# Performance work log

Hardware: AMD Instinct MI355X
Metric: run time of the kernel (lower is better)

The kernel has to match this reference:

```python
import jax, jax.numpy as jnp
import numpy as np

NEG_SLOPE = 0.2
EPS = 1e-16
N_NODES = 50000
N_EDGES = 800000
D_IN = 128
D_E = 64
HEADS = 4
D_OUT = 32


def setup_inputs() -> dict:
    key = jax.random.key(0)
    k1, k2, k3, k4, k5, k6 = jax.random.split(key, 6)
    H = jax.random.normal(k1, (N_NODES, D_IN), dtype=jnp.float32)
    edge_index = jax.random.randint(k2, (2, N_EDGES), 0, N_NODES, dtype=jnp.int64)
    E = jax.random.normal(k3, (N_EDGES, D_E), dtype=jnp.float32)
    # torch nn.Linear weights: [out_features, in_features]
    W = jax.random.normal(k4, (HEADS * D_OUT, D_IN), dtype=jnp.float32) * (1.0 / np.sqrt(D_IN))
    W_e = jax.random.normal(k5, (HEADS * D_OUT, D_E), dtype=jnp.float32) * (1.0 / np.sqrt(D_E))
    att = jax.random.normal(k6, (1, HEADS, D_OUT), dtype=jnp.float32) * 0.1
    return {"H": H, "edge_index": edge_index, "E": E, "W": W, "W_e": W_e, "att": att}


def reference(H, edge_index, E, W, W_e, att):
    n_nodes = H.shape[0]
    # node transform: [N, heads, d_out]
    HT = (H @ W.T).reshape(n_nodes, HEADS, D_OUT)
    src, dst = edge_index[0], edge_index[1]
    # edge transform: [E, heads, d_out]
    ET = (E @ W_e.T).reshape(-1, HEADS, D_OUT)
    alpha_in = HT[src] + HT[dst] + ET              # [E, heads, d_out]
    alpha_in = jax.nn.leaky_relu(alpha_in, NEG_SLOPE)
    alpha = jnp.sum(alpha_in * att, axis=-1)        # [E, heads]
    # segment softmax over incoming edges of each dst node
    a_max = jax.ops.segment_max(alpha, dst, num_segments=n_nodes)   # [N, heads]
    alpha = jnp.exp(alpha - a_max[dst])
    a_sum = jax.ops.segment_sum(alpha, dst, num_segments=n_nodes)   # [N, heads]
    alpha = alpha / (a_sum[dst] + EPS)
    # weighted aggregation of source features
    messages = HT[src] * alpha[:, :, None]          # [E, heads, d_out]
    H_out = jax.ops.segment_sum(messages, dst, num_segments=n_nodes)  # [N, heads, d_out]
    return H_out.reshape(n_nodes, HEADS * D_OUT)    # concat=True
```

## Files before the change

kernel.cpp:

```cpp
#include <hip/hip_runtime.h>

#define N_NODES 50000
#define N_EDGES 800000
#define D_IN    128
#define D_E     64
#define NH      4
#define F_TOT   128
#define NEG_SLOPE 0.2f

typedef __attribute__((ext_vector_type(8))) short short8;
typedef __attribute__((ext_vector_type(4))) float f32x4;

__device__ __forceinline__ short f2bf(float x) {
    unsigned u = __float_as_uint(x);
    u += 0x7FFFu + ((u >> 16) & 1u);
    return (short)(u >> 16);
}

__global__ __launch_bounds__(256) void k_node_transform(
    const float* __restrict__ H, const float* __restrict__ W,
    float* __restrict__ HT)
{
    __shared__ float wt[D_IN * F_TOT];
    const int tid = threadIdx.x;
    for (int i = tid; i < D_IN * F_TOT; i += 256) {
        const int f = i & 127, k = i >> 7;
        wt[k * F_TOT + f] = W[f * D_IN + k];
    }
    __syncthreads();

    const int l = tid & 63;
    const int w = tid >> 6;
    const int gwave  = blockIdx.x * 4 + w;
    const int nwaves = gridDim.x * 4;
    const int ngroups = N_NODES / 8;

    for (int grp = gwave; grp < ngroups; grp += nwaves) {
        const int g = grp * 8;
        float ax[8], ay[8];
#pragma unroll
        for (int j = 0; j < 8; ++j) { ax[j] = 0.f; ay[j] = 0.f; }

        for (int k4 = 0; k4 < D_IN / 4; ++k4) {
            float hv[8][4];
#pragma unroll
            for (int j = 0; j < 8; ++j)
                *(float4*)hv[j] = *(const float4*)&H[(size_t)(g + j) * D_IN + k4 * 4];
#pragma unroll
            for (int kk = 0; kk < 4; ++kk) {
                const float2 wk = *(const float2*)&wt[(k4 * 4 + kk) * F_TOT + 2 * l];
#pragma unroll
                for (int j = 0; j < 8; ++j) {
                    ax[j] = fmaf(wk.x, hv[j][kk], ax[j]);
                    ay[j] = fmaf(wk.y, hv[j][kk], ay[j]);
                }
            }
        }
#pragma unroll
        for (int j = 0; j < 8; ++j) {
            float2 r; r.x = ax[j]; r.y = ay[j];
            *(float2*)&HT[(size_t)(g + j) * F_TOT + 2 * l] = r;
        }
    }
}

__global__ __launch_bounds__(256) void k_hist(
    const int* __restrict__ EI, int* __restrict__ deg)
{
    const int e = blockIdx.x * 256 + threadIdx.x;
    if (e < N_EDGES) atomicAdd(&deg[EI[N_EDGES + e]], 1);
}

__global__ __launch_bounds__(1024) void k_scan(
    const int* __restrict__ deg, int* __restrict__ row_start,
    int* __restrict__ cursor)
{
    __shared__ int wsum[16];
    __shared__ int carry;
    const int tid = threadIdx.x;
    const int l = tid & 63;
    const int wv = tid >> 6;
    if (tid == 0) carry = 0;

    for (int base = 0; base < N_NODES; base += 1024) {
        __syncthreads();
        const int cb = carry;
        const int i = base + tid;
        const int v = (i < N_NODES) ? deg[i] : 0;
        int x = v;
#pragma unroll
        for (int off = 1; off < 64; off <<= 1) {
            int t = __shfl_up(x, off, 64);
            if (l >= off) x += t;
        }
        if (l == 63) wsum[wv] = x;
        __syncthreads();
        int wave_off = 0;
        for (int k = 0; k < wv; ++k) wave_off += wsum[k];
        int tot = 0;
#pragma unroll
        for (int k = 0; k < 16; ++k) tot += wsum[k];
        const int excl = cb + wave_off + (x - v);
        if (i < N_NODES) { row_start[i] = excl; cursor[i] = excl; }
        __syncthreads();
        if (tid == 0) carry = cb + tot;
    }
    __syncthreads();
    if (tid == 0) row_start[N_NODES] = carry;
}

__global__ __launch_bounds__(256, 3) void k_logits(
    const float* __restrict__ E, const int* __restrict__ EI,
    const float* __restrict__ We, const float* __restrict__ att,
    const float* __restrict__ HT,
    float* __restrict__ wperm, int* __restrict__ srcperm,
    int* __restrict__ cursor)
{
    const int tid = threadIdx.x;
    const int l   = tid & 63;
    const int wv  = tid >> 6;
    const int r16 = l & 15;
    const int g4  = l >> 4;

    short8 bf[8][2];
#pragma unroll
    for (int ft = 0; ft < 8; ++ft) {
#pragma unroll
        for (int kc = 0; kc < 2; ++kc) {
            const float* wp = &We[(size_t)(ft * 16 + r16) * D_E + kc * 32 + g4 * 8];
            const float4 lo = *(const float4*)wp;
            const float4 hi = *(const float4*)(wp + 4);
            short8 b;
            b[0] = f2bf(lo.x); b[1] = f2bf(lo.y); b[2] = f2bf(lo.z); b[3] = f2bf(lo.w);
            b[4] = f2bf(hi.x); b[5] = f2bf(hi.y); b[6] = f2bf(hi.z); b[7] = f2bf(hi.w);
            bf[ft][kc] = b;
        }
    }
    float attv[8];
#pragma unroll
    for (int ft = 0; ft < 8; ++ft) attv[ft] = att[ft * 16 + r16];

    const int gwave  = blockIdx.x * 4 + wv;
    const int nwaves = gridDim.x * 4;
    const int ntiles = N_EDGES / 16;

    for (int t = gwave; t < ntiles; t += nwaves) {
        const int e0 = t * 16;
        short8 af[2];
#pragma unroll
        for (int kc = 0; kc < 2; ++kc) {
            const float* ep = &E[(size_t)(e0 + r16) * D_E + kc * 32 + g4 * 8];
            const float4 lo = *(const float4*)ep;
            const float4 hi = *(const float4*)(ep + 4);
            short8 a;
            a[0] = f2bf(lo.x); a[1] = f2bf(lo.y); a[2] = f2bf(lo.z); a[3] = f2bf(lo.w);
            a[4] = f2bf(hi.x); a[5] = f2bf(hi.y); a[6] = f2bf(hi.z); a[7] = f2bf(hi.w);
            af[kc] = a;
        }
        f32x4 acc[8];
#pragma unroll
        for (int ft = 0; ft < 8; ++ft) {
            f32x4 z = {0.f, 0.f, 0.f, 0.f};
            z = __builtin_amdgcn_mfma_f32_16x16x32_bf16(af[0], bf[ft][0], z, 0, 0, 0);
            acc[ft] = __builtin_amdgcn_mfma_f32_16x16x32_bf16(af[1], bf[ft][1], z, 0, 0, 0);
        }
        int sr_[4], dr_[4];
#pragma unroll
        for (int r = 0; r < 4; ++r) {
            sr_[r] = EI[e0 + g4 * 4 + r];
            dr_[r] = EI[N_EDGES + e0 + g4 * 4 + r];
        }
#pragma unroll
        for (int r = 0; r < 4; ++r) {
            const int sr = sr_[r], dr = dr_[r];
            float ph[4] = {0.f, 0.f, 0.f, 0.f};
#pragma unroll
            for (int ft = 0; ft < 8; ++ft) {
                const float hs = HT[(size_t)sr * F_TOT + ft * 16 + r16];
                const float hd = HT[(size_t)dr * F_TOT + ft * 16 + r16];
                float v = hs + hd + acc[ft][r];
                v = v > 0.f ? v : NEG_SLOPE * v;
                ph[ft >> 1] = fmaf(v, attv[ft], ph[ft >> 1]);
            }
#pragma unroll
            for (int m = 1; m < 16; m <<= 1) {
#pragma unroll
                for (int hh = 0; hh < 4; ++hh)
                    ph[hh] += __shfl_xor(ph[hh], m, 64);
            }
            const float w0 = __expf(ph[0]), w1 = __expf(ph[1]);
            const float w2 = __expf(ph[2]), w3 = __expf(ph[3]);
            int pos = 0;
            if (r16 == 0) pos = atomicAdd(&cursor[dr], 1);
            pos = __shfl(pos, l & 48, 64);
            if (r16 < 4) {
                const float wv_ = r16 == 0 ? w0 : r16 == 1 ? w1 : r16 == 2 ? w2 : w3;
                wperm[4 * pos + r16] = wv_;
            }
            if (r16 == 4) srcperm[pos] = sr;
        }
    }
}

__global__ __launch_bounds__(256, 8) void k_aggregate(
    const float* __restrict__ HT, const float* __restrict__ wperm,
    const int* __restrict__ srcperm, const int* __restrict__ row_start,
    float* __restrict__ out)
{
    const int tid = threadIdx.x;
    const int l = tid & 63;
    const int wv = tid >> 6;
    const int n = blockIdx.x * 4 + wv;
    if (n >= N_NODES) return;
    const int h = l >> 4;
    const int beg = row_start[n];
    const int end = row_start[n + 1];

    float ax = 0.f, ay = 0.f, sw = 0.f;
    for (int base = beg; base < end; base += 16) {
        const int   svl = (l < 16 && base + l < end) ? srcperm[base + l] : 0;
        const float wvl = (4 * base + l < 4 * end) ? wperm[4 * base + l] : 0.f;
#pragma unroll
        for (int j = 0; j < 16; ++j) {
            const int   s = __shfl(svl, j, 64);
            const float w = __shfl(wvl, 4 * j + h, 64);
            const float2 hs = *(const float2*)&HT[(size_t)s * F_TOT + 2 * l];
            ax = fmaf(w, hs.x, ax);
            ay = fmaf(w, hs.y, ay);
            sw += w;
        }
    }
    const float inv = 1.f / (sw + 1e-16f);
    float2 r; r.x = ax * inv; r.y = ay * inv;
    *(float2*)&out[(size_t)n * F_TOT + 2 * l] = r;
}

extern "C" void kernel_launch(void* const* d_in, const int* in_sizes, int n_in,
                              void* d_out, int out_size, void* d_ws, size_t ws_size,
                              hipStream_t stream)
{
    const float* H   = (const float*)d_in[0];
    const int*   EI  = (const int*)d_in[1];
    const float* E   = (const float*)d_in[2];
    const float* W   = (const float*)d_in[3];
    const float* We  = (const float*)d_in[4];
    const float* att = (const float*)d_in[5];
    float* out = (float*)d_out;

    float* HT        = (float*)d_ws;
    float* wperm     = HT + (size_t)N_NODES * F_TOT;
    int*   srcperm   = (int*)(wperm + (size_t)N_EDGES * NH);
    int*   deg       = srcperm + N_EDGES;
    int*   row_start = deg + N_NODES;
    int*   cursor    = row_start + N_NODES + 1;

    hipMemsetAsync(deg, 0, N_NODES * sizeof(int), stream);

    k_hist<<<(N_EDGES + 255) / 256, 256, 0, stream>>>(EI, deg);
    k_scan<<<1, 1024, 0, stream>>>(deg, row_start, cursor);
    k_node_transform<<<512, 256, 0, stream>>>(H, W, HT);
    k_logits<<<1024, 256, 0, stream>>>(E, EI, We, att, HT,
                                       wperm, srcperm, cursor);
    k_aggregate<<<(N_NODES + 3) / 4, 256, 0, stream>>>(HT, wperm, srcperm,
                                                       row_start, out);
}
```

Measured before the change: 687.3 us.

## Fuse edge logits and aggregation into per-destination-node kernel with swizzled HT

Edges are now bucketed by destination in a separate permute kernel that stores source and edge ids. A single per-node kernel then computes the edge transform via MFMA, the logits, the exponentials and the weighted aggregation, so the wperm buffer and the second gather of HT are gone. HT columns are stored in a swizzled order so each lane loads 8 contiguous floats with vector loads, and the destination row is loaded once per node. The trade-off is that E rows are now gathered in random order, degree imbalance across waves, and MFMA tiles are partly wasted on nodes whose degree is not a multiple of 16.

```diff
diff --git a/kernel.cpp b/kernel.cpp
--- a/kernel.cpp
+++ b/kernel.cpp
@@ -19,13 +19,14 @@
 
 __global__ __launch_bounds__(256) void k_node_transform(
     const float* __restrict__ H, const float* __restrict__ W,
-    float* __restrict__ HT)
+    float* __restrict__ HTsw)
 {
     __shared__ float wt[D_IN * F_TOT];
     const int tid = threadIdx.x;
     for (int i = tid; i < D_IN * F_TOT; i += 256) {
-        const int f = i & 127, k = i >> 7;
-        wt[k * F_TOT + f] = W[f * D_IN + k];
+        const int s = i & 127, k = i >> 7;
+        const int f = (s & 7) * 16 + (s >> 3);
+        wt[k * F_TOT + s] = W[f * D_IN + k];
     }
     __syncthreads();
 
@@ -59,7 +60,7 @@
 #pragma unroll
         for (int j = 0; j < 8; ++j) {
             float2 r; r.x = ax[j]; r.y = ay[j];
-            *(float2*)&HT[(size_t)(g + j) * F_TOT + 2 * l] = r;
+            *(float2*)&HTsw[(size_t)(g + j) * F_TOT + 2 * l] = r;
         }
     }
 }
@@ -109,12 +110,25 @@
     if (tid == 0) row_start[N_NODES] = carry;
 }
 
-__global__ __launch_bounds__(256, 3) void k_logits(
-    const float* __restrict__ E, const int* __restrict__ EI,
-    const float* __restrict__ We, const float* __restrict__ att,
-    const float* __restrict__ HT,
-    float* __restrict__ wperm, int* __restrict__ srcperm,
-    int* __restrict__ cursor)
+__global__ __launch_bounds__(256) void k_permute(
+    const int* __restrict__ EI, int* __restrict__ cursor,
+    int* __restrict__ srcperm, int* __restrict__ eidperm)
+{
+    const int e = blockIdx.x * 256 + threadIdx.x;
+    if (e < N_EDGES) {
+        const int s = EI[e];
+        const int d = EI[N_EDGES + e];
+        const int pos = atomicAdd(&cursor[d], 1);
+        srcperm[pos] = s;
+        eidperm[pos] = e;
+    }
+}
+
+__global__ __launch_bounds__(256, 3) void k_gat(
+    const float* __restrict__ E, const float* __restrict__ We,
+    const float* __restrict__ att, const float* __restrict__ HTsw,
+    const int* __restrict__ srcperm, const int* __restrict__ eidperm,
+    const int* __restrict__ row_start, float* __restrict__ out)
 {
     const int tid = threadIdx.x;
     const int l   = tid & 63;
@@ -140,45 +154,74 @@
 #pragma unroll
     for (int ft = 0; ft < 8; ++ft) attv[ft] = att[ft * 16 + r16];
 
-    const int gwave  = blockIdx.x * 4 + wv;
-    const int nwaves = gridDim.x * 4;
-    const int ntiles = N_EDGES / 16;
-
-    for (int t = gwave; t < ntiles; t += nwaves) {
-        const int e0 = t * 16;
-        short8 af[2];
-#pragma unroll
-        for (int kc = 0; kc < 2; ++kc) {
-            const float* ep = &E[(size_t)(e0 + r16) * D_E + kc * 32 + g4 * 8];
-            const float4 lo = *(const float4*)ep;
-            const float4 hi = *(const float4*)(ep + 4);
-            short8 a;
-            a[0] = f2bf(lo.x); a[1] = f2bf(lo.y); a[2] = f2bf(lo.z); a[3] = f2bf(lo.w);
-            a[4] = f2bf(hi.x); a[5] = f2bf(hi.y); a[6] = f2bf(hi.z); a[7] = f2bf(hi.w);
-            af[kc] = a;
-        }
+    const int n = blockIdx.x * 4 + wv;
+    if (n >= N_NODES) return;
+    const int beg = row_start[n];
+    const int end = row_start[n + 1];
+
+    float hdv[8];
+    {
+        const float4 d0 = *(const float4*)&HTsw[(size_t)n * F_TOT + r16 * 8];
+        const float4 d1 = *(const float4*)&HTsw[(size_t)n * F_TOT + r16 * 8 + 4];
+        hdv[0] = d0.x; hdv[1] = d0.y; hdv[2] = d0.z; hdv[3] = d0.w;
+        hdv[4] = d1.x; hdv[5] = d1.y; hdv[6] = d1.z; hdv[7] = d1.w;
+    }
+
+    float macc[8];
+#pragma unroll
+    for (int ft = 0; ft < 8; ++ft) macc[ft] = 0.f;
+    float sw4[4] = {0.f, 0.f, 0.f, 0.f};
+
+    for (int base = beg; base < end; base += 16) {
+        int svl = 0, evl = 0;
+        if (l < 16) {
+            const int idx = base + l;
+            const int cidx = idx < end ? idx : beg;
+            svl = srcperm[cidx];
+            evl = eidperm[cidx];
+        }
+        const int eid = __shfl(evl, r16, 64);
+        const float* ep = &E[(size_t)eid * D_E + g4 * 8];
+        const float4 a0 = *(const float4*)ep;
+        const float4 a1 = *(const float4*)(ep + 4);
+        const float4 a2 = *(const float4*)(ep + 32);
+        const float4 a3 = *(const float4*)(ep + 36);
+
+        int sidx[4];
+#pragma unroll
+        for (int r = 0; r < 4; ++r) sidx[r] = __shfl(svl, g4 * 4 + r, 64);
+        float4 h0[4], h1[4];
+#pragma unroll
+        for (int r = 0; r < 4; ++r) {
+            const float* hp = &HTsw[(size_t)sidx[r] * F_TOT + r16 * 8];
+            h0[r] = *(const float4*)hp;
+            h1[r] = *(const float4*)(hp + 4);
+        }
+
+        short8 af0, af1;
+        af0[0] = f2bf(a0.x); af0[1] = f2bf(a0.y); af0[2] = f2bf(a0.z); af0[3] = f2bf(a0.w);
+        af0[4] = f2bf(a1.x); af0[5] = f2bf(a1.y); af0[6] = f2bf(a1.z); af0[7] = f2bf(a1.w);
+        af1[0] = f2bf(a2.x); af1[1] = f2bf(a2.y); af1[2] = f2bf(a2.z); af1[3] = f2bf(a2.w);
+        af1[4] = f2bf(a3.x); af1[5] = f2bf(a3.y); af1[6] = f2bf(a3.z); af1[7] = f2bf(a3.w);
+
         f32x4 acc[8];
 #pragma unroll
         for (int ft = 0; ft < 8; ++ft) {
             f32x4 z = {0.f, 0.f, 0.f, 0.f};
-            z = __builtin_amdgcn_mfma_f32_16x16x32_bf16(af[0], bf[ft][0], z, 0, 0, 0);
-            acc[ft] = __builtin_amdgcn_mfma_f32_16x16x32_bf16(af[1], bf[ft][1], z, 0, 0, 0);
-        }
-        int sr_[4], dr_[4];
+            z = __builtin_amdgcn_mfma_f32_16x16x32_bf16(af0, bf[ft][0], z, 0, 0, 0);
+            acc[ft] = __builtin_amdgcn_mfma_f32_16x16x32_bf16(af1, bf[ft][1], z, 0, 0, 0);
+        }
+
 #pragma unroll
         for (int r = 0; r < 4; ++r) {
-            sr_[r] = EI[e0 + g4 * 4 + r];
-            dr_[r] = EI[N_EDGES + e0 + g4 * 4 + r];
-        }
-#pragma unroll
-        for (int r = 0; r < 4; ++r) {
-            const int sr = sr_[r], dr = dr_[r];
+            const bool valid = (base + g4 * 4 + r) < end;
+            float hsv[8];
+            hsv[0] = h0[r].x; hsv[1] = h0[r].y; hsv[2] = h0[r].z; hsv[3] = h0[r].w;
+            hsv[4] = h1[r].x; hsv[5] = h1[r].y; hsv[6] = h1[r].z; hsv[7] = h1[r].w;
             float ph[4] = {0.f, 0.f, 0.f, 0.f};
 #pragma unroll
             for (int ft = 0; ft < 8; ++ft) {
-                const float hs = HT[(size_t)sr * F_TOT + ft * 16 + r16];
-                const float hd = HT[(size_t)dr * F_TOT + ft * 16 + r16];
-                float v = hs + hd + acc[ft][r];
+                float v = hsv[ft] + hdv[ft] + acc[ft][r];
                 v = v > 0.f ? v : NEG_SLOPE * v;
                 ph[ft >> 1] = fmaf(v, attv[ft], ph[ft >> 1]);
             }
@@ -188,51 +231,29 @@
                 for (int hh = 0; hh < 4; ++hh)
                     ph[hh] += __shfl_xor(ph[hh], m, 64);
             }
-            const float w0 = __expf(ph[0]), w1 = __expf(ph[1]);
-            const float w2 = __expf(ph[2]), w3 = __expf(ph[3]);
-            int pos = 0;
-            if (r16 == 0) pos = atomicAdd(&cursor[dr], 1);
-            pos = __shfl(pos, l & 48, 64);
-            if (r16 < 4) {
-                const float wv_ = r16 == 0 ? w0 : r16 == 1 ? w1 : r16 == 2 ? w2 : w3;
-                wperm[4 * pos + r16] = wv_;
-            }
-            if (r16 == 4) srcperm[pos] = sr;
-        }
-    }
-}
-
-__global__ __launch_bounds__(256, 8) void k_aggregate(
-    const float* __restrict__ HT, const float* __restrict__ wperm,
-    const int* __restrict__ srcperm, const int* __restrict__ row_start,
-    float* __restrict__ out)
-{
-    const int tid = threadIdx.x;
-    const int l = tid & 63;
-    const int wv = tid >> 6;
-    const int n = blockIdx.x * 4 + wv;
-    if (n >= N_NODES) return;
-    const int h = l >> 4;
-    const int beg = row_start[n];
-    const int end = row_start[n + 1];
-
-    float ax = 0.f, ay = 0.f, sw = 0.f;
-    for (int base = beg; base < end; base += 16) {
-        const int   svl = (l < 16 && base + l < end) ? srcperm[base + l] : 0;
-        const float wvl = (4 * base + l < 4 * end) ? wperm[4 * base + l] : 0.f;
-#pragma unroll
-        for (int j = 0; j < 16; ++j) {
-            const int   s = __shfl(svl, j, 64);
-            const float w = __shfl(wvl, 4 * j + h, 64);
-            const float2 hs = *(const float2*)&HT[(size_t)s * F_TOT + 2 * l];
-            ax = fmaf(w, hs.x, ax);
-            ay = fmaf(w, hs.y, ay);
-            sw += w;
-        }
-    }
-    const float inv = 1.f / (sw + 1e-16f);
-    float2 r; r.x = ax * inv; r.y = ay * inv;
-    *(float2*)&out[(size_t)n * F_TOT + 2 * l] = r;
+            float wgt[4];
+#pragma unroll
+            for (int hh = 0; hh < 4; ++hh)
+                wgt[hh] = valid ? __expf(ph[hh]) : 0.f;
+#pragma unroll
+            for (int ft = 0; ft < 8; ++ft)
+                macc[ft] = fmaf(wgt[ft >> 1], hsv[ft], macc[ft]);
+#pragma unroll
+            for (int hh = 0; hh < 4; ++hh) sw4[hh] += wgt[hh];
+        }
+    }
+
+#pragma unroll
+    for (int mask = 16; mask < 64; mask <<= 1) {
+#pragma unroll
+        for (int ft = 0; ft < 8; ++ft) macc[ft] += __shfl_xor(macc[ft], mask, 64);
+#pragma unroll
+        for (int hh = 0; hh < 4; ++hh) sw4[hh] += __shfl_xor(sw4[hh], mask, 64);
+    }
+    const float inv = 1.f / (sw4[g4] + 1e-16f);
+    const int f0 = (2 * g4) * 16 + r16;
+    out[(size_t)n * F_TOT + f0]      = macc[2 * g4]     * inv;
+    out[(size_t)n * F_TOT + f0 + 16] = macc[2 * g4 + 1] * inv;
 }
 
 extern "C" void kernel_launch(void* const* d_in, const int* in_sizes, int n_in,
@@ -247,10 +268,10 @@
     const float* att = (const float*)d_in[5];
     float* out = (float*)d_out;
 
-    float* HT        = (float*)d_ws;
-    float* wperm     = HT + (size_t)N_NODES * F_TOT;
-    int*   srcperm   = (int*)(wperm + (size_t)N_EDGES * NH);
-    int*   deg       = srcperm + N_EDGES;
+    float* HTsw      = (float*)d_ws;
+    int*   srcperm   = (int*)(HTsw + (size_t)N_NODES * F_TOT);
+    int*   eidperm   = srcperm + N_EDGES;
+    int*   deg       = eidperm + N_EDGES;
     int*   row_start = deg + N_NODES;
     int*   cursor    = row_start + N_NODES + 1;
 
@@ -258,9 +279,10 @@
 
     k_hist<<<(N_EDGES + 255) / 256, 256, 0, stream>>>(EI, deg);
     k_scan<<<1, 1024, 0, stream>>>(deg, row_start, cursor);
-    k_node_transform<<<512, 256, 0, stream>>>(H, W, HT);
-    k_logits<<<1024, 256, 0, stream>>>(E, EI, We, att, HT,
-                                       wperm, srcperm, cursor);
-    k_aggregate<<<(N_NODES + 3) / 4, 256, 0, stream>>>(HT, wperm, srcperm,
-                                                       row_start, out);
-}
+    k_node_transform<<<512, 256, 0, stream>>>(H, W, HTsw);
+    k_permute<<<(N_EDGES + 255) / 256, 256, 0, stream>>>(EI, cursor,
+                                                         srcperm, eidperm);
+    k_gat<<<(N_NODES + 3) / 4, 256, 0, stream>>>(E, We, att, HTsw,
+                                                 srcperm, eidperm,
+                                                 row_start, out);
+}
```

After: 781.2 us. +13.7%, slower.
